# Kernel optimization log

Hardware: AMD Instinct MI355X
Metric: run time of the kernel (lower is better)

Reference implementation:

```python
import jax, jax.numpy as jnp
import numpy as np

PATCH = 16

def setup_inputs() -> dict:
    key = jax.random.key(0)
    batch = jax.random.normal(key, (3, 1280, 1280), dtype=jnp.float32)
    return {"batch": batch}

def reference(batch) -> jnp.ndarray:
    # batch: (3, H, W). Torch forward unsqueezes to (1,3,H,W) -> bs=1.
    C, H, W = batch.shape
    ps = PATCH
    hp, wp = H // ps, W // ps
    N = hp * wp
    # unfold(1,3,3).unfold(2,ps,ps).unfold(3,ps,ps) -> (1,1,hp,wp,3,ps,ps)
    # -> reshape to (1,hp,wp,3,ps,ps); here flatten to (N, 3, ps*ps)
    patches = batch.reshape(C, hp, ps, wp, ps).transpose(1, 3, 0, 2, 4)  # (hp,wp,3,ps,ps)
    feats = patches.reshape(N, C, ps * ps)
    # per-patch channel gram, divided by d*e*f = 3*ps*ps
    G = jnp.einsum('nce,nde->ncd', feats, feats) / (C * ps * ps)  # (N,3,3)
    Gf = G.reshape(N, C * C)  # (N,9)
    # pairwise MSE: mean((Gg-Gn)^2) = (|Gg|^2 + |Gn|^2 - 2<Gg,Gn>) / 9
    sq = jnp.sum(Gf * Gf, axis=1)              # (N,)
    inner = Gf @ Gf.T                           # (N,N) GEMM, K=9
    dist = (sq[:, None] + sq[None, :] - 2.0 * inner) / (C * C)
    # per-image normalization: subtract min, then divide by (new) max
    dist = dist - jnp.min(dist)
    dist = dist / jnp.max(dist)
    return dist[None]  # (1, N, N)
```

## Files before the change

kernel.cpp:

```cpp
#include <hip/hip_runtime.h>

#define PS 16
#define HW 1280
#define NPS 80
#define NP (NPS * NPS)
#define GS 12

typedef float vf4 __attribute__((ext_vector_type(4)));

__device__ __forceinline__ unsigned f2ord(float f) {
    unsigned u = __float_as_uint(f);
    return (u & 0x80000000u) ? ~u : (u | 0x80000000u);
}
__device__ __forceinline__ float ord2f(unsigned m) {
    return (m & 0x80000000u) ? __uint_as_float(m & 0x7FFFFFFFu) : __uint_as_float(~m);
}

__global__ __launch_bounds__(256) void gram_kernel(const float* __restrict__ x,
                                                   float* __restrict__ G,
                                                   unsigned* __restrict__ mm) {
    const int t = threadIdx.x;
    if (blockIdx.x == 0 && t == 0) mm[0] = 0u;
    const int n = blockIdx.x * 4 + (t >> 6);
    const int l = t & 63;
    const int pi = n / NPS, pj = n % NPS;
    const int r = l >> 2, c = (l & 3) * 4;
    const size_t base = (size_t)(pi * PS + r) * HW + pj * PS + c;
    const float4 A = *(const float4*)(x + base);
    const float4 B = *(const float4*)(x + base + (size_t)HW * HW);
    const float4 C = *(const float4*)(x + base + 2 * (size_t)HW * HW);
    float p[6];
    p[0] = A.x * A.x + A.y * A.y + A.z * A.z + A.w * A.w;
    p[1] = A.x * B.x + A.y * B.y + A.z * B.z + A.w * B.w;
    p[2] = A.x * C.x + A.y * C.y + A.z * C.z + A.w * C.w;
    p[3] = B.x * B.x + B.y * B.y + B.z * B.z + B.w * B.w;
    p[4] = B.x * C.x + B.y * C.y + B.z * C.z + B.w * C.w;
    p[5] = C.x * C.x + C.y * C.y + C.z * C.z + C.w * C.w;
#pragma unroll
    for (int k = 0; k < 6; ++k) {
        float v = p[k];
#pragma unroll
        for (int off = 32; off; off >>= 1) v += __shfl_xor(v, off);
        p[k] = v;
    }
    if (l == 0) {
        const float sc = 1.0f / 768.0f;
        const float g0 = p[0] * sc, g1 = p[1] * sc, g2 = p[2] * sc;
        const float g3 = p[3] * sc, g4 = p[4] * sc, g5 = p[5] * sc;
        const float row[9] = {g0, g1, g2, g1, g3, g4, g2, g4, g5};
        float s = 0.f;
#pragma unroll
        for (int k = 0; k < 9; ++k) s = fmaf(row[k], row[k], s);
        float* dst = G + (size_t)n * GS;
        *(float4*)(dst)     = make_float4(row[0], row[1], row[2], row[3]);
        *(float4*)(dst + 4) = make_float4(row[4], row[5], row[6], row[7]);
        *(float4*)(dst + 8) = make_float4(row[8], s, 0.f, 0.f);
    }
}

#define MI 64
#define MJ 256
__global__ __launch_bounds__(256) void max_kernel(const float* __restrict__ G,
                                                  unsigned* __restrict__ mm) {
    const int i0 = blockIdx.x * MI;
    const int j0 = blockIdx.y * MJ;
    if (i0 > j0 + MJ - 1) return;
    __shared__ float rg[MI * GS];
    __shared__ float smax[4];
    const int t = threadIdx.x;
    if (t < MI * GS / 4)
        ((float4*)rg)[t] = *(const float4*)(G + (size_t)i0 * GS + t * 4);
    __syncthreads();
    const int l = t & 63, w = t >> 6;
    const int j = j0 + l * 4;
    float gj[4][10];
#pragma unroll
    for (int c = 0; c < 4; ++c) {
        const float* src = G + (size_t)(j + c) * GS;
        const float4 a = *(const float4*)(src);
        const float4 b = *(const float4*)(src + 4);
        const float4 q = *(const float4*)(src + 8);
        gj[c][0] = a.x; gj[c][1] = a.y; gj[c][2] = a.z; gj[c][3] = a.w;
        gj[c][4] = b.x; gj[c][5] = b.y; gj[c][6] = b.z; gj[c][7] = b.w;
        gj[c][8] = q.x; gj[c][9] = q.y;
    }
    float vmax = -3.4e38f;
#pragma unroll 4
    for (int rr = 0; rr < MI / 4; ++rr) {
        const int r = w * (MI / 4) + rr;
        const float4 a = *(const float4*)(rg + r * GS);
        const float4 b = *(const float4*)(rg + r * GS + 4);
        const float4 q = *(const float4*)(rg + r * GS + 8);
        const float gi[9] = {a.x, a.y, a.z, a.w, b.x, b.y, b.z, b.w, q.x};
        const float si = q.y;
#pragma unroll
        for (int c = 0; c < 4; ++c) {
            float inner = 0.f;
#pragma unroll
            for (int k = 0; k < 9; ++k) inner = fmaf(gi[k], gj[c][k], inner);
            vmax = fmaxf(vmax, si + gj[c][9] - 2.f * inner);
        }
    }
#pragma unroll
    for (int off = 32; off; off >>= 1) vmax = fmaxf(vmax, __shfl_xor(vmax, off));
    if ((t & 63) == 0) smax[w] = vmax;
    __syncthreads();
    if (t == 0) {
        const float bmax = fmaxf(fmaxf(smax[0], smax[1]), fmaxf(smax[2], smax[3]));
        atomicMax(mm, f2ord(bmax));
    }
}

#define WI 16
__global__ __launch_bounds__(320) void write_kernel(const float* __restrict__ G,
                                                    const unsigned* __restrict__ mm,
                                                    float* __restrict__ out) {
    const int t = threadIdx.x;
    const int w = t >> 6, l = t & 63;
    const int i0 = blockIdx.y * WI;
    const int jw = blockIdx.x * 1280 + w * 256 + l * 4;
    __shared__ float rg[WI * GS];
    if (t < WI * GS / 4)
        ((float4*)rg)[t] = *(const float4*)(G + (size_t)i0 * GS + t * 4);
    float gj[4][10];
#pragma unroll
    for (int c = 0; c < 4; ++c) {
        const float* src = G + (size_t)(jw + c) * GS;
        const float4 a = *(const float4*)(src);
        const float4 b = *(const float4*)(src + 4);
        const float4 q = *(const float4*)(src + 8);
        gj[c][0] = a.x; gj[c][1] = a.y; gj[c][2] = a.z; gj[c][3] = a.w;
        gj[c][4] = b.x; gj[c][5] = b.y; gj[c][6] = b.z; gj[c][7] = b.w;
        gj[c][8] = q.x; gj[c][9] = q.y;
    }
    const float inv = 1.f / ord2f(mm[0]);
    __syncthreads();
    float* dst = out + (size_t)i0 * NP + jw;
#pragma unroll 4
    for (int rr = 0; rr < WI; ++rr) {
        const float4 a = *(const float4*)(rg + rr * GS);
        const float4 b = *(const float4*)(rg + rr * GS + 4);
        const float4 q = *(const float4*)(rg + rr * GS + 8);
        const float gi[9] = {a.x, a.y, a.z, a.w, b.x, b.y, b.z, b.w, q.x};
        const float si = q.y;
        vf4 dv;
#pragma unroll
        for (int c = 0; c < 4; ++c) {
            float inner = 0.f;
#pragma unroll
            for (int k = 0; k < 9; ++k) inner = fmaf(gi[k], gj[c][k], inner);
            dv[c] = (si + gj[c][9] - 2.f * inner) * inv;
        }
        *(vf4*)dst = dv;
        dst += NP;
    }
}

extern "C" void kernel_launch(void* const* d_in, const int* in_sizes, int n_in,
                              void* d_out, int out_size, void* d_ws, size_t ws_size,
                              hipStream_t stream) {
    (void)in_sizes; (void)n_in; (void)out_size; (void)ws_size;
    const float* x = (const float*)d_in[0];
    float* out = (float*)d_out;
    float* G = (float*)d_ws;
    unsigned* mm = (unsigned*)((char*)d_ws + (size_t)NP * GS * sizeof(float));

    gram_kernel<<<NP / 4, 256, 0, stream>>>(x, G, mm);
    max_kernel<<<dim3(NP / MI, NP / MJ), 256, 0, stream>>>(G, mm);
    write_kernel<<<dim3(5, NP / WI), 320, 0, stream>>>(G, mm, out);
}
```

Before: 59.80 us.

## Fuse max and write kernels into persistent kernel with grid barrier

Replaces the separate max-reduction and output-write kernels with one persistent kernel of 512 blocks. Each block loops over tiles to compute a partial max, publishes it with an atomic, and spins on a global counter until every block has arrived. It then revisits the same tiles to write the normalized output. This removes one kernel launch and its gap, but adds a spin-wait grid barrier that assumes all 512 blocks are resident at once, and it changes the tile shapes for both phases.

```diff
diff --git a/kernel.cpp b/kernel.cpp
--- a/kernel.cpp
+++ b/kernel.cpp
@@ -5,6 +5,13 @@
 #define NPS 80
 #define NP (NPS * NPS)
 #define GS 12
+
+#define FBLK 512
+#define TI 64
+#define TJW 1280
+#define NBI (NP / TI)
+#define NBJ (NP / TJW)
+#define NTILE (NBI * NBJ)
 
 typedef float vf4 __attribute__((ext_vector_type(4)));
 
@@ -18,9 +25,10 @@
 
 __global__ __launch_bounds__(256) void gram_kernel(const float* __restrict__ x,
                                                    float* __restrict__ G,
-                                                   unsigned* __restrict__ mm) {
+                                                   unsigned* __restrict__ mm,
+                                                   unsigned* __restrict__ bar) {
     const int t = threadIdx.x;
-    if (blockIdx.x == 0 && t == 0) mm[0] = 0u;
+    if (blockIdx.x == 0 && t == 0) { mm[0] = 0u; bar[0] = 0u; }
     const int n = blockIdx.x * 4 + (t >> 6);
     const int l = t & 63;
     const int pi = n / NPS, pj = n % NPS;
@@ -58,101 +66,110 @@
     }
 }
 
-#define MI 64
-#define MJ 256
-__global__ __launch_bounds__(256) void max_kernel(const float* __restrict__ G,
-                                                  unsigned* __restrict__ mm) {
-    const int i0 = blockIdx.x * MI;
-    const int j0 = blockIdx.y * MJ;
-    if (i0 > j0 + MJ - 1) return;
-    __shared__ float rg[MI * GS];
-    __shared__ float smax[4];
+__global__ __launch_bounds__(320, 4) void maxwrite_kernel(const float* __restrict__ G,
+                                                          unsigned* __restrict__ mm,
+                                                          unsigned* __restrict__ bar,
+                                                          float* __restrict__ out) {
     const int t = threadIdx.x;
-    if (t < MI * GS / 4)
-        ((float4*)rg)[t] = *(const float4*)(G + (size_t)i0 * GS + t * 4);
-    __syncthreads();
-    const int l = t & 63, w = t >> 6;
-    const int j = j0 + l * 4;
-    float gj[4][10];
-#pragma unroll
-    for (int c = 0; c < 4; ++c) {
-        const float* src = G + (size_t)(j + c) * GS;
-        const float4 a = *(const float4*)(src);
-        const float4 b = *(const float4*)(src + 4);
-        const float4 q = *(const float4*)(src + 8);
-        gj[c][0] = a.x; gj[c][1] = a.y; gj[c][2] = a.z; gj[c][3] = a.w;
-        gj[c][4] = b.x; gj[c][5] = b.y; gj[c][6] = b.z; gj[c][7] = b.w;
-        gj[c][8] = q.x; gj[c][9] = q.y;
-    }
+    const int w = t >> 6, l = t & 63;
+    __shared__ float rg[TI * GS];
+    __shared__ float smax[5];
+    __shared__ float sinv;
+
     float vmax = -3.4e38f;
-#pragma unroll 4
-    for (int rr = 0; rr < MI / 4; ++rr) {
-        const int r = w * (MI / 4) + rr;
-        const float4 a = *(const float4*)(rg + r * GS);
-        const float4 b = *(const float4*)(rg + r * GS + 4);
-        const float4 q = *(const float4*)(rg + r * GS + 8);
-        const float gi[9] = {a.x, a.y, a.z, a.w, b.x, b.y, b.z, b.w, q.x};
-        const float si = q.y;
+    for (int tau = blockIdx.x; tau < NTILE; tau += FBLK) {
+        const int bi = tau / NBJ, bj = tau % NBJ;
+        const int i0 = bi * TI, j0 = bj * TJW;
+        if (i0 > j0 + TJW - 1) continue;
+        __syncthreads();
+        if (t < TI * GS / 4)
+            ((float4*)rg)[t] = *(const float4*)(G + (size_t)i0 * GS + t * 4);
+        __syncthreads();
+        const int jw = j0 + w * 256 + l * 4;
+        float gj[4][10];
 #pragma unroll
         for (int c = 0; c < 4; ++c) {
-            float inner = 0.f;
+            const float* src = G + (size_t)(jw + c) * GS;
+            const float4 a = *(const float4*)(src);
+            const float4 b = *(const float4*)(src + 4);
+            const float4 q = *(const float4*)(src + 8);
+            gj[c][0] = a.x; gj[c][1] = a.y; gj[c][2] = a.z; gj[c][3] = a.w;
+            gj[c][4] = b.x; gj[c][5] = b.y; gj[c][6] = b.z; gj[c][7] = b.w;
+            gj[c][8] = q.x; gj[c][9] = q.y;
+        }
+#pragma unroll 4
+        for (int r = 0; r < TI; ++r) {
+            const float4 a = *(const float4*)(rg + r * GS);
+            const float4 b = *(const float4*)(rg + r * GS + 4);
+            const float4 q = *(const float4*)(rg + r * GS + 8);
+            const float gi[9] = {a.x, a.y, a.z, a.w, b.x, b.y, b.z, b.w, q.x};
+            const float si = q.y;
 #pragma unroll
-            for (int k = 0; k < 9; ++k) inner = fmaf(gi[k], gj[c][k], inner);
-            vmax = fmaxf(vmax, si + gj[c][9] - 2.f * inner);
+            for (int c = 0; c < 4; ++c) {
+                float inner = 0.f;
+#pragma unroll
+                for (int k = 0; k < 9; ++k) inner = fmaf(gi[k], gj[c][k], inner);
+                vmax = fmaxf(vmax, si + gj[c][9] - 2.f * inner);
+            }
         }
     }
 #pragma unroll
     for (int off = 32; off; off >>= 1) vmax = fmaxf(vmax, __shfl_xor(vmax, off));
-    if ((t & 63) == 0) smax[w] = vmax;
+    if (l == 0) smax[w] = vmax;
     __syncthreads();
+
     if (t == 0) {
-        const float bmax = fmaxf(fmaxf(smax[0], smax[1]), fmaxf(smax[2], smax[3]));
-        atomicMax(mm, f2ord(bmax));
+        float bm = fmaxf(fmaxf(fmaxf(smax[0], smax[1]), fmaxf(smax[2], smax[3])), smax[4]);
+        atomicMax(mm, f2ord(bm));
+        __threadfence();
+        atomicAdd(bar, 1u);
+        unsigned v;
+        do {
+            v = __hip_atomic_load(bar, __ATOMIC_ACQUIRE, __HIP_MEMORY_SCOPE_AGENT);
+        } while (v < FBLK);
+        sinv = 1.0f / ord2f(atomicOr(mm, 0u));
     }
-}
+    __syncthreads();
+    const float inv = sinv;
 
-#define WI 16
-__global__ __launch_bounds__(320) void write_kernel(const float* __restrict__ G,
-                                                    const unsigned* __restrict__ mm,
-                                                    float* __restrict__ out) {
-    const int t = threadIdx.x;
-    const int w = t >> 6, l = t & 63;
-    const int i0 = blockIdx.y * WI;
-    const int jw = blockIdx.x * 1280 + w * 256 + l * 4;
-    __shared__ float rg[WI * GS];
-    if (t < WI * GS / 4)
-        ((float4*)rg)[t] = *(const float4*)(G + (size_t)i0 * GS + t * 4);
-    float gj[4][10];
-#pragma unroll
-    for (int c = 0; c < 4; ++c) {
-        const float* src = G + (size_t)(jw + c) * GS;
-        const float4 a = *(const float4*)(src);
-        const float4 b = *(const float4*)(src + 4);
-        const float4 q = *(const float4*)(src + 8);
-        gj[c][0] = a.x; gj[c][1] = a.y; gj[c][2] = a.z; gj[c][3] = a.w;
-        gj[c][4] = b.x; gj[c][5] = b.y; gj[c][6] = b.z; gj[c][7] = b.w;
-        gj[c][8] = q.x; gj[c][9] = q.y;
-    }
-    const float inv = 1.f / ord2f(mm[0]);
-    __syncthreads();
-    float* dst = out + (size_t)i0 * NP + jw;
-#pragma unroll 4
-    for (int rr = 0; rr < WI; ++rr) {
-        const float4 a = *(const float4*)(rg + rr * GS);
-        const float4 b = *(const float4*)(rg + rr * GS + 4);
-        const float4 q = *(const float4*)(rg + rr * GS + 8);
-        const float gi[9] = {a.x, a.y, a.z, a.w, b.x, b.y, b.z, b.w, q.x};
-        const float si = q.y;
-        vf4 dv;
+    for (int tau = blockIdx.x; tau < NTILE; tau += FBLK) {
+        const int bi = tau / NBJ, bj = tau % NBJ;
+        const int i0 = bi * TI, j0 = bj * TJW;
+        __syncthreads();
+        if (t < TI * GS / 4)
+            ((float4*)rg)[t] = *(const float4*)(G + (size_t)i0 * GS + t * 4);
+        __syncthreads();
+        const int jw = j0 + w * 256 + l * 4;
+        float gj[4][10];
 #pragma unroll
         for (int c = 0; c < 4; ++c) {
-            float inner = 0.f;
+            const float* src = G + (size_t)(jw + c) * GS;
+            const float4 a = *(const float4*)(src);
+            const float4 b = *(const float4*)(src + 4);
+            const float4 q = *(const float4*)(src + 8);
+            gj[c][0] = a.x; gj[c][1] = a.y; gj[c][2] = a.z; gj[c][3] = a.w;
+            gj[c][4] = b.x; gj[c][5] = b.y; gj[c][6] = b.z; gj[c][7] = b.w;
+            gj[c][8] = q.x; gj[c][9] = q.y;
+        }
+        float* dst = out + (size_t)i0 * NP + jw;
+#pragma unroll 4
+        for (int r = 0; r < TI; ++r) {
+            const float4 a = *(const float4*)(rg + r * GS);
+            const float4 b = *(const float4*)(rg + r * GS + 4);
+            const float4 q = *(const float4*)(rg + r * GS + 8);
+            const float gi[9] = {a.x, a.y, a.z, a.w, b.x, b.y, b.z, b.w, q.x};
+            const float si = q.y;
+            vf4 dv;
 #pragma unroll
-            for (int k = 0; k < 9; ++k) inner = fmaf(gi[k], gj[c][k], inner);
-            dv[c] = (si + gj[c][9] - 2.f * inner) * inv;
+            for (int c = 0; c < 4; ++c) {
+                float inner = 0.f;
+#pragma unroll
+                for (int k = 0; k < 9; ++k) inner = fmaf(gi[k], gj[c][k], inner);
+                dv[c] = (si + gj[c][9] - 2.f * inner) * inv;
+            }
+            *(vf4*)dst = dv;
+            dst += NP;
         }
-        *(vf4*)dst = dv;
-        dst += NP;
     }
 }
 
@@ -164,8 +181,8 @@
     float* out = (float*)d_out;
     float* G = (float*)d_ws;
     unsigned* mm = (unsigned*)((char*)d_ws + (size_t)NP * GS * sizeof(float));
+    unsigned* bar = mm + 1;
 
-    gram_kernel<<<NP / 4, 256, 0, stream>>>(x, G, mm);
-    max_kernel<<<dim3(NP / MI, NP / MJ), 256, 0, stream>>>(G, mm);
-    write_kernel<<<dim3(5, NP / WI), 320, 0, stream>>>(G, mm, out);
+    gram_kernel<<<NP / 4, 256, 0, stream>>>(x, G, mm, bar);
+    maxwrite_kernel<<<FBLK, 320, 0, stream>>>(G, mm, bar, out);
 }
```

Result: slower. 120.9 us (+102.2%).

## Compute global distance max with bf16 MFMA on augmented Gram vectors

Applied to the files above, without the earlier changes.

The Gram kernel now also writes bf16 augmented vectors U=[-2g, |g|^2, 1] and V=[g, 1, |g|^2], so a single 32x32x16 bf16 MFMA gives a whole tile of squared distances. The scalar FMA max kernel is replaced by a grid-stride MFMA kernel that reduces each tile to a maximum. It now covers the full matrix instead of the upper triangle, and the write kernel processes 32 rows per block instead of 16. The aim is to cut the ALU cost of the max pass. The risk is that the bf16 rounding and cancellation in the max may shift the normalisation constant away from the fp32 reference.

```diff
diff --git a/kernel.cpp b/kernel.cpp
--- a/kernel.cpp
+++ b/kernel.cpp
@@ -5,8 +5,11 @@
 #define NPS 80
 #define NP (NPS * NPS)
 #define GS 12
+#define NT32 (NP / 32)
 
 typedef float vf4 __attribute__((ext_vector_type(4)));
+typedef short bf16x8 __attribute__((ext_vector_type(8)));
+typedef float f32x16 __attribute__((ext_vector_type(16)));
 
 __device__ __forceinline__ unsigned f2ord(float f) {
     unsigned u = __float_as_uint(f);
@@ -15,9 +18,15 @@
 __device__ __forceinline__ float ord2f(unsigned m) {
     return (m & 0x80000000u) ? __uint_as_float(m & 0x7FFFFFFFu) : __uint_as_float(~m);
 }
+__device__ __forceinline__ unsigned short f2bf(float f) {
+    unsigned u = __float_as_uint(f);
+    return (unsigned short)((u + 0x7FFFu + ((u >> 16) & 1u)) >> 16);
+}
 
 __global__ __launch_bounds__(256) void gram_kernel(const float* __restrict__ x,
                                                    float* __restrict__ G,
+                                                   unsigned short* __restrict__ U,
+                                                   unsigned short* __restrict__ V,
                                                    unsigned* __restrict__ mm) {
     const int t = threadIdx.x;
     if (blockIdx.x == 0 && t == 0) mm[0] = 0u;
@@ -55,63 +64,60 @@
         *(float4*)(dst)     = make_float4(row[0], row[1], row[2], row[3]);
         *(float4*)(dst + 4) = make_float4(row[4], row[5], row[6], row[7]);
         *(float4*)(dst + 8) = make_float4(row[8], s, 0.f, 0.f);
+        unsigned short u16[16], v16[16];
+#pragma unroll
+        for (int k = 0; k < 9; ++k) { u16[k] = f2bf(-2.f * row[k]); v16[k] = f2bf(row[k]); }
+        const unsigned short one = f2bf(1.0f), sb = f2bf(s);
+        u16[9] = sb;  u16[10] = one;
+        v16[9] = one; v16[10] = sb;
+#pragma unroll
+        for (int k = 11; k < 16; ++k) { u16[k] = 0; v16[k] = 0; }
+        uint4 uw, vw;
+        uw.x = u16[0] | (u16[1] << 16); uw.y = u16[2] | (u16[3] << 16);
+        uw.z = u16[4] | (u16[5] << 16); uw.w = u16[6] | (u16[7] << 16);
+        *(uint4*)(U + (size_t)n * 16) = uw;
+        uw.x = u16[8] | (u16[9] << 16); uw.y = u16[10] | (u16[11] << 16);
+        uw.z = 0; uw.w = 0;
+        *(uint4*)(U + (size_t)n * 16 + 8) = uw;
+        vw.x = v16[0] | (v16[1] << 16); vw.y = v16[2] | (v16[3] << 16);
+        vw.z = v16[4] | (v16[5] << 16); vw.w = v16[6] | (v16[7] << 16);
+        *(uint4*)(V + (size_t)n * 16) = vw;
+        vw.x = v16[8] | (v16[9] << 16); vw.y = v16[10] | (v16[11] << 16);
+        vw.z = 0; vw.w = 0;
+        *(uint4*)(V + (size_t)n * 16 + 8) = vw;
     }
 }
 
-#define MI 64
-#define MJ 256
-__global__ __launch_bounds__(256) void max_kernel(const float* __restrict__ G,
-                                                  unsigned* __restrict__ mm) {
-    const int i0 = blockIdx.x * MI;
-    const int j0 = blockIdx.y * MJ;
-    if (i0 > j0 + MJ - 1) return;
-    __shared__ float rg[MI * GS];
-    __shared__ float smax[4];
+#define MMB 2048
+__global__ __launch_bounds__(256) void mfma_max_kernel(const unsigned short* __restrict__ U,
+                                                       const unsigned short* __restrict__ V,
+                                                       unsigned* __restrict__ mm) {
     const int t = threadIdx.x;
-    if (t < MI * GS / 4)
-        ((float4*)rg)[t] = *(const float4*)(G + (size_t)i0 * GS + t * 4);
-    __syncthreads();
-    const int l = t & 63, w = t >> 6;
-    const int j = j0 + l * 4;
-    float gj[4][10];
+    const int w = t >> 6, l = t & 63;
+    const int wid = blockIdx.x * 4 + w;
+    const int row = l & 31, kg = l >> 5;
+    float vmax = -3.4e38f;
+    const f32x16 zero = {0.f};
+    for (int wt = wid; wt < NT32 * NT32; wt += MMB * 4) {
+        const int ti = wt / NT32, tj = wt % NT32;
+        const bf16x8 a = *(const bf16x8*)(U + (size_t)(ti * 32 + row) * 16 + kg * 8);
+        const bf16x8 b = *(const bf16x8*)(V + (size_t)(tj * 32 + row) * 16 + kg * 8);
+        const f32x16 d = __builtin_amdgcn_mfma_f32_32x32x16_bf16(a, b, zero, 0, 0, 0);
 #pragma unroll
-    for (int c = 0; c < 4; ++c) {
-        const float* src = G + (size_t)(j + c) * GS;
-        const float4 a = *(const float4*)(src);
-        const float4 b = *(const float4*)(src + 4);
-        const float4 q = *(const float4*)(src + 8);
-        gj[c][0] = a.x; gj[c][1] = a.y; gj[c][2] = a.z; gj[c][3] = a.w;
-        gj[c][4] = b.x; gj[c][5] = b.y; gj[c][6] = b.z; gj[c][7] = b.w;
-        gj[c][8] = q.x; gj[c][9] = q.y;
-    }
-    float vmax = -3.4e38f;
-#pragma unroll 4
-    for (int rr = 0; rr < MI / 4; ++rr) {
-        const int r = w * (MI / 4) + rr;
-        const float4 a = *(const float4*)(rg + r * GS);
-        const float4 b = *(const float4*)(rg + r * GS + 4);
-        const float4 q = *(const float4*)(rg + r * GS + 8);
-        const float gi[9] = {a.x, a.y, a.z, a.w, b.x, b.y, b.z, b.w, q.x};
-        const float si = q.y;
-#pragma unroll
-        for (int c = 0; c < 4; ++c) {
-            float inner = 0.f;
-#pragma unroll
-            for (int k = 0; k < 9; ++k) inner = fmaf(gi[k], gj[c][k], inner);
-            vmax = fmaxf(vmax, si + gj[c][9] - 2.f * inner);
-        }
+        for (int k = 0; k < 16; ++k) vmax = fmaxf(vmax, d[k]);
     }
 #pragma unroll
     for (int off = 32; off; off >>= 1) vmax = fmaxf(vmax, __shfl_xor(vmax, off));
-    if ((t & 63) == 0) smax[w] = vmax;
+    __shared__ float smax[4];
+    if (l == 0) smax[w] = vmax;
     __syncthreads();
     if (t == 0) {
-        const float bmax = fmaxf(fmaxf(smax[0], smax[1]), fmaxf(smax[2], smax[3]));
-        atomicMax(mm, f2ord(bmax));
+        const float bm = fmaxf(fmaxf(smax[0], smax[1]), fmaxf(smax[2], smax[3]));
+        atomicMax(mm, f2ord(bm));
     }
 }
 
-#define WI 16
+#define WI 32
 __global__ __launch_bounds__(320) void write_kernel(const float* __restrict__ G,
                                                     const unsigned* __restrict__ mm,
                                                     float* __restrict__ out) {
@@ -162,10 +168,13 @@
     (void)in_sizes; (void)n_in; (void)out_size; (void)ws_size;
     const float* x = (const float*)d_in[0];
     float* out = (float*)d_out;
-    float* G = (float*)d_ws;
-    unsigned* mm = (unsigned*)((char*)d_ws + (size_t)NP * GS * sizeof(float));
+    char* ws = (char*)d_ws;
+    float* G = (float*)ws;
+    unsigned short* U = (unsigned short*)(ws + 307200);
+    unsigned short* V = (unsigned short*)(ws + 512000);
+    unsigned* mm = (unsigned*)(ws + 716800);
 
-    gram_kernel<<<NP / 4, 256, 0, stream>>>(x, G, mm);
-    max_kernel<<<dim3(NP / MI, NP / MJ), 256, 0, stream>>>(G, mm);
+    gram_kernel<<<NP / 4, 256, 0, stream>>>(x, G, U, V, mm);
+    mfma_max_kernel<<<MMB, 256, 0, stream>>>(U, V, mm);
     write_kernel<<<dim3(5, NP / WI), 320, 0, stream>>>(G, mm, out);
 }
```

Measured after the change: 67.92 us. +13.6%, slower.
